# Kernel optimization log

Measured on AMD Instinct MI355X. Metric: run time of the kernel, lower is better.

The kernel has to match this reference:

```python
import jax, jax.numpy as jnp
import numpy as np

B, CTX_DIM, CTX_SIZE, HID, SEQLEN = 32, 1024, 2048, 1024, 64


def setup_inputs() -> dict:
    key = jax.random.key(0)
    k1, k2, k3, k4 = jax.random.split(key, 4)
    hidden = jax.random.normal(k1, (1, B, HID), dtype=jnp.float32)
    contextvects = jax.random.normal(k2, (B, CTX_DIM, CTX_SIZE), dtype=jnp.float32)
    # nn.Linear(context_dim, hidden_size): W is [hidden_size, context_dim]
    W = jax.random.normal(k3, (HID, CTX_DIM), dtype=jnp.float32) / np.sqrt(CTX_DIM)
    b = jax.random.normal(k4, (HID,), dtype=jnp.float32) * 0.01
    return {"seqlen": SEQLEN, "hidden": hidden, "contextvects": contextvects, "W": W, "b": b}


def reference(seqlen, hidden, contextvects, W, b):
    # Original torch loop recomputes the identical quantities every timestep;
    # compute once and broadcast across seqlen (same math, no redundancy).
    # contextvects: [B, D, C]; project each context position: [B, C, H]
    context_proj = jnp.einsum('bdc,hd->bch', contextvects, W) + b
    # hidden: [1, B, H] -> scores [B, C]
    scores = jnp.einsum('bch,bh->bc', context_proj, hidden[0])
    attn_weights = jax.nn.softmax(scores, axis=1)  # softmax over context positions
    ctx = jnp.einsum('bdc,bc->bd', contextvects, attn_weights)  # [B, D]
    return jnp.broadcast_to(ctx[None, :, :], (seqlen, ctx.shape[0], ctx.shape[1]))
```

## Files before the change

kernel.cpp:

```cpp
#include <hip/hip_runtime.h>
#include <math.h>

#define NB 32
#define ND 1024
#define NC 2048
#define NH 1024
#define NSEQ 64
#define CCHUNK 32
#define NCHUNK (NC / CCHUNK)

__global__ __launch_bounds__(256) void k1_v(const float* __restrict__ hidden,
                                            const float* __restrict__ W,
                                            float* __restrict__ v) {
  __shared__ float part[128];
  const int b = blockIdx.x >> 3;
  const int dl = threadIdx.x & 127;
  const int d = ((blockIdx.x & 7) << 7) + dl;
  const int hh = threadIdx.x >> 7;
  const float* hb = hidden + b * NH + hh * 512;
  const float* Wp = W + (size_t)hh * 512 * ND + d;
  float acc = 0.f;
#pragma unroll 16
  for (int h = 0; h < 512; ++h) acc += hb[h] * Wp[(size_t)h * ND];
  if (hh) part[dl] = acc;
  __syncthreads();
  if (!hh) v[b * ND + d] = acc + part[dl];
}

__global__ __launch_bounds__(512, 4) void k2_main(const float* __restrict__ ctx,
                                                  const float* __restrict__ v,
                                                  float* __restrict__ accp,
                                                  float* __restrict__ ml) {
  __shared__ __align__(16) float sred[64 * 32];
  __shared__ float pf[CCHUNK];

  const int t = threadIdx.x;
  const int bid = blockIdx.x;
  const int b = bid >> 6;
  const int c0 = (bid & (NCHUNK - 1)) << 5;
  const int dp = t >> 3;
  const int cg = t & 7;

  const float* g = ctx + (size_t)b * ND * NC + (size_t)dp * NC + c0 + (cg << 2);
  float4 x[16];
#pragma unroll
  for (int j = 0; j < 16; ++j) x[j] = *(const float4*)(g + (size_t)j * (64 * NC));

  float vsr[16];
  const float* vb = v + b * ND + dp;
#pragma unroll
  for (int j = 0; j < 16; ++j) vsr[j] = vb[j * 64];

  float4 s4 = make_float4(0.f, 0.f, 0.f, 0.f);
#pragma unroll
  for (int j = 0; j < 16; ++j) {
    const float vd = vsr[j];
    s4.x += x[j].x * vd; s4.y += x[j].y * vd;
    s4.z += x[j].z * vd; s4.w += x[j].w * vd;
  }
  *(float4*)(sred + 4 * t) = s4;
  __syncthreads();

  if (t < 32) {
    float s = 0.f;
#pragma unroll
    for (int q = 0; q < 64; ++q) s += sred[32 * q + t];
    float mm = s;
#pragma unroll
    for (int off = 16; off; off >>= 1) mm = fmaxf(mm, __shfl_xor(mm, off, 32));
    float e = __expf(s - mm);
    float l = e;
#pragma unroll
    for (int off = 16; off; off >>= 1) l += __shfl_xor(l, off, 32);
    pf[t] = e;
    if (t == 0) { ml[bid * 2] = mm; ml[bid * 2 + 1] = l; }
  }
  __syncthreads();

  const float4 p4 = *(const float4*)(pf + (cg << 2));
  float* ao = accp + (size_t)bid * ND;
#pragma unroll
  for (int j = 0; j < 16; ++j) {
    float aj = x[j].x * p4.x + x[j].y * p4.y + x[j].z * p4.z + x[j].w * p4.w;
    aj += __shfl_xor(aj, 1, 64);
    aj += __shfl_xor(aj, 2, 64);
    aj += __shfl_xor(aj, 4, 64);
    if (cg == (j & 7)) ao[dp + (j << 6)] = aj;
  }
}

__global__ __launch_bounds__(128) void k3_combine_bcast(
    const float* __restrict__ accp, const float* __restrict__ ml,
    float* __restrict__ out) {
  __shared__ float sc[NCHUNK];
  __shared__ float sinv_s;
  const int b = blockIdx.x >> 3;
  const int dslice = blockIdx.x & 7;
  const int t = threadIdx.x;

  if (t < NCHUNK) {
    float mi = ml[(b * NCHUNK + t) * 2];
    float li = ml[(b * NCHUNK + t) * 2 + 1];
    float mg = mi;
#pragma unroll
    for (int off = 32; off; off >>= 1) mg = fmaxf(mg, __shfl_xor(mg, off, 64));
    float scale = __expf(mi - mg);
    float dpart = scale * li;
#pragma unroll
    for (int off = 32; off; off >>= 1) dpart += __shfl_xor(dpart, off, 64);
    sc[t] = scale;
    if (t == 0) sinv_s = 1.0f / dpart;
  }
  __syncthreads();
  const float sinv = sinv_s;

  const int d = dslice * 128 + t;
  const float* ap = accp + (size_t)b * NCHUNK * ND + d;
  float acc = 0.f;
#pragma unroll 16
  for (int i = 0; i < NCHUNK; ++i) acc += sc[i] * ap[(size_t)i * ND];
  acc *= sinv;

  float* op = out + b * ND + d;
#pragma unroll 8
  for (int s = 0; s < NSEQ; ++s) op[(size_t)s * NB * ND] = acc;
}

extern "C" void kernel_launch(void* const* d_in, const int* in_sizes, int n_in,
                              void* d_out, int out_size, void* d_ws, size_t ws_size,
                              hipStream_t stream) {
  (void)in_sizes; (void)n_in; (void)out_size; (void)ws_size;
  const float* hidden = (const float*)d_in[1];
  const float* ctxv   = (const float*)d_in[2];
  const float* W      = (const float*)d_in[3];
  float* out = (float*)d_out;

  char* ws = (char*)d_ws;
  float* v    = (float*)(ws);
  float* ml   = (float*)(ws + 131072);
  float* accp = (float*)(ws + 131072 + 16384);

  k1_v<<<256, 256, 0, stream>>>(hidden, W, v);
  k2_main<<<NB * NCHUNK, 512, 0, stream>>>(ctxv, v, accp, ml);
  k3_combine_bcast<<<256, 128, 0, stream>>>(accp, ml, out);
}
```

Baseline: 403.8 us.

## Use nontemporal loads/stores, split k1 over 4 H-quarters, split k3 broadcast across seq halves

k1 now uses 512 threads, so each thread sums a quarter of the hidden dimension and three partial sums are reduced through shared memory. k2 loads the context tensor with nontemporal loads and uses ext_vector_type arithmetic. k3 launches twice as many blocks, each writing half of the sequence broadcast with nontemporal stores. The aim is more parallelism in the small kernels and less cache pollution from streaming traffic, at the cost of recomputing the combine step in both halves.

```diff
diff --git a/kernel.cpp b/kernel.cpp
--- a/kernel.cpp
+++ b/kernel.cpp
@@ -9,22 +9,24 @@
 #define CCHUNK 32
 #define NCHUNK (NC / CCHUNK)
 
-__global__ __launch_bounds__(256) void k1_v(const float* __restrict__ hidden,
+typedef float v4f __attribute__((ext_vector_type(4)));
+
+__global__ __launch_bounds__(512) void k1_v(const float* __restrict__ hidden,
                                             const float* __restrict__ W,
                                             float* __restrict__ v) {
-  __shared__ float part[128];
+  __shared__ float part[3][128];
   const int b = blockIdx.x >> 3;
   const int dl = threadIdx.x & 127;
   const int d = ((blockIdx.x & 7) << 7) + dl;
   const int hh = threadIdx.x >> 7;
-  const float* hb = hidden + b * NH + hh * 512;
-  const float* Wp = W + (size_t)hh * 512 * ND + d;
+  const float* hb = hidden + b * NH + hh * 256;
+  const float* Wp = W + (size_t)(hh * 256) * ND + d;
   float acc = 0.f;
 #pragma unroll 16
-  for (int h = 0; h < 512; ++h) acc += hb[h] * Wp[(size_t)h * ND];
-  if (hh) part[dl] = acc;
+  for (int h = 0; h < 256; ++h) acc += hb[h] * Wp[(size_t)h * ND];
+  if (hh) part[hh - 1][dl] = acc;
   __syncthreads();
-  if (!hh) v[b * ND + d] = acc + part[dl];
+  if (!hh) v[b * ND + d] = acc + part[0][dl] + part[1][dl] + part[2][dl];
 }
 
 __global__ __launch_bounds__(512, 4) void k2_main(const float* __restrict__ ctx,
@@ -42,23 +44,20 @@
   const int cg = t & 7;
 
   const float* g = ctx + (size_t)b * ND * NC + (size_t)dp * NC + c0 + (cg << 2);
-  float4 x[16];
+  v4f x[16];
 #pragma unroll
-  for (int j = 0; j < 16; ++j) x[j] = *(const float4*)(g + (size_t)j * (64 * NC));
+  for (int j = 0; j < 16; ++j)
+    x[j] = __builtin_nontemporal_load((const v4f*)(g + (size_t)j * (64 * NC)));
 
   float vsr[16];
   const float* vb = v + b * ND + dp;
 #pragma unroll
   for (int j = 0; j < 16; ++j) vsr[j] = vb[j * 64];
 
-  float4 s4 = make_float4(0.f, 0.f, 0.f, 0.f);
+  v4f s4 = (v4f)(0.f);
 #pragma unroll
-  for (int j = 0; j < 16; ++j) {
-    const float vd = vsr[j];
-    s4.x += x[j].x * vd; s4.y += x[j].y * vd;
-    s4.z += x[j].z * vd; s4.w += x[j].w * vd;
-  }
-  *(float4*)(sred + 4 * t) = s4;
+  for (int j = 0; j < 16; ++j) s4 += x[j] * vsr[j];
+  *(v4f*)(sred + 4 * t) = s4;
   __syncthreads();
 
   if (t < 32) {
@@ -77,11 +76,12 @@
   }
   __syncthreads();
 
-  const float4 p4 = *(const float4*)(pf + (cg << 2));
+  const v4f p4 = *(const v4f*)(pf + (cg << 2));
   float* ao = accp + (size_t)bid * ND;
 #pragma unroll
   for (int j = 0; j < 16; ++j) {
-    float aj = x[j].x * p4.x + x[j].y * p4.y + x[j].z * p4.z + x[j].w * p4.w;
+    v4f m4 = x[j] * p4;
+    float aj = m4.x + m4.y + m4.z + m4.w;
     aj += __shfl_xor(aj, 1, 64);
     aj += __shfl_xor(aj, 2, 64);
     aj += __shfl_xor(aj, 4, 64);
@@ -94,8 +94,9 @@
     float* __restrict__ out) {
   __shared__ float sc[NCHUNK];
   __shared__ float sinv_s;
-  const int b = blockIdx.x >> 3;
-  const int dslice = blockIdx.x & 7;
+  const int b = blockIdx.x >> 4;
+  const int dslice = (blockIdx.x >> 1) & 7;
+  const int shalf = blockIdx.x & 1;
   const int t = threadIdx.x;
 
   if (t < NCHUNK) {
@@ -121,9 +122,10 @@
   for (int i = 0; i < NCHUNK; ++i) acc += sc[i] * ap[(size_t)i * ND];
   acc *= sinv;
 
-  float* op = out + b * ND + d;
+  float* op = out + b * ND + d + (size_t)shalf * (NSEQ / 2) * NB * ND;
 #pragma unroll 8
-  for (int s = 0; s < NSEQ; ++s) op[(size_t)s * NB * ND] = acc;
+  for (int s = 0; s < NSEQ / 2; ++s)
+    __builtin_nontemporal_store(acc, op + (size_t)s * NB * ND);
 }
 
 extern "C" void kernel_launch(void* const* d_in, const int* in_sizes, int n_in,
@@ -140,7 +142,7 @@
   float* ml   = (float*)(ws + 131072);
   float* accp = (float*)(ws + 131072 + 16384);
 
-  k1_v<<<256, 256, 0, stream>>>(hidden, W, v);
+  k1_v<<<256, 512, 0, stream>>>(hidden, W, v);
   k2_main<<<NB * NCHUNK, 512, 0, stream>>>(ctxv, v, accp, ml);
-  k3_combine_bcast<<<256, 128, 0, stream>>>(accp, ml, out);
+  k3_combine_bcast<<<512, 128, 0, stream>>>(accp, ml, out);
 }
```

Measured after the change: 373.7 us (median of 2 runs). 1.08x faster.
